# Kernel optimization log

Hardware: AMD Instinct MI355X
Metric: run time of the kernel (lower is better)

## Reference

```python
import jax, jax.numpy as jnp
import numpy as np

EMB = 64
NUM_LAYERS = 2


def _mlp_embed(x, shift, scale, w1, b1, w2, b2):
    # PreNormLayer: (x + shift) * scale, then Linear-ReLU-Linear-ReLU
    x = (x + shift) * scale
    x = jax.nn.relu(x @ w1 + b1)
    return jax.nn.relu(x @ w2 + b2)


def _sage_conv(x_src, x_dst, src_idx, dst_idx, ll_w, ll_b, lr_w):
    # PyG SAGEConv: mean-aggregate gathered source features at destinations,
    # out = lin_l(mean) + lin_r(x_dst); lin_l has bias, lin_r does not.
    n_dst = x_dst.shape[0]
    msgs = x_src[src_idx]                                   # [E, D] gather
    ssum = jax.ops.segment_sum(msgs, dst_idx, num_segments=n_dst)
    cnt = jax.ops.segment_sum(jnp.ones(src_idx.shape[0], x_src.dtype),
                              dst_idx, num_segments=n_dst)
    mean = ssum / jnp.maximum(cnt, 1.0)[:, None]            # [n_dst, D]
    return mean @ ll_w + ll_b + x_dst @ lr_w


def setup_inputs() -> dict:
    key = jax.random.key(0)
    ks = jax.random.split(key, 20)
    n_cons, n_var, n_edges = 100_000, 200_000, 2_000_000
    cons_nf, var_nf, edge_nf = 5, 19, 1

    def lin(k, fan_in, fan_out):
        return jax.random.normal(k, (fan_in, fan_out), jnp.float32) / np.sqrt(fan_in)

    inp = {
        'cons_x': jax.random.normal(ks[0], (n_cons, cons_nf), jnp.float32),
        'var_x': jax.random.normal(ks[1], (n_var, var_nf), jnp.float32),
        'edge_attr': jax.random.normal(ks[2], (n_edges, edge_nf), jnp.float32),
        'edge_index': jnp.stack([
            jax.random.randint(ks[3], (n_edges,), 0, n_cons),
            jax.random.randint(ks[4], (n_edges,), 0, n_var)]).astype(jnp.int64),
        # constraint embedding MLP
        'cons_shift': 0.1 * jax.random.normal(ks[5], (cons_nf,), jnp.float32),
        'cons_scale': 1.0 + 0.1 * jax.random.normal(ks[6], (cons_nf,), jnp.float32),
        'cons_w1': lin(ks[7], cons_nf, EMB),
        'cons_b1': jnp.zeros((EMB,), jnp.float32),
        'cons_w2': lin(ks[8], EMB, EMB),
        'cons_b2': jnp.zeros((EMB,), jnp.float32),
        # variable embedding MLP
        'var_shift': 0.1 * jax.random.normal(ks[9], (var_nf,), jnp.float32),
        'var_scale': 1.0 + 0.1 * jax.random.normal(ks[10], (var_nf,), jnp.float32),
        'var_w1': lin(ks[11], var_nf, EMB),
        'var_b1': jnp.zeros((EMB,), jnp.float32),
        'var_w2': lin(ks[12], EMB, EMB),
        'var_b2': jnp.zeros((EMB,), jnp.float32),
        # edge PreNorm (computed but unused for conv_type='sage', as in source)
        'edge_shift': 0.1 * jax.random.normal(ks[13], (edge_nf,), jnp.float32),
        'edge_scale': 1.0 + 0.1 * jax.random.normal(ks[14], (edge_nf,), jnp.float32),
        # SAGEConv weights: [layer, direction(0: cons->var, 1: var->cons), in, out]
        'conv_ll_w': jax.random.normal(ks[15], (NUM_LAYERS, 2, EMB, EMB), jnp.float32) / np.sqrt(EMB),
        'conv_ll_b': jnp.zeros((NUM_LAYERS, 2, EMB), jnp.float32),
        'conv_lr_w': jax.random.normal(ks[16], (NUM_LAYERS, 2, EMB, EMB), jnp.float32) / np.sqrt(EMB),
    }
    return inp


def reference(cons_x, var_x, edge_attr, edge_index,
              cons_shift, cons_scale, cons_w1, cons_b1, cons_w2, cons_b2,
              var_shift, var_scale, var_w1, var_b1, var_w2, var_b2,
              edge_shift, edge_scale, conv_ll_w, conv_ll_b, conv_lr_w):
    x_c = _mlp_embed(cons_x, cons_shift, cons_scale, cons_w1, cons_b1, cons_w2, cons_b2)
    x_v = _mlp_embed(var_x, var_shift, var_scale, var_w1, var_b1, var_w2, var_b2)
    edge_feat = (edge_attr + edge_shift) * edge_scale  # unused for SAGE (faithful to source)
    del edge_feat
    src, dst = edge_index[0], edge_index[1]  # constraint -> variable
    for l in range(NUM_LAYERS):
        new_v = _sage_conv(x_c, x_v, src, dst, conv_ll_w[l, 0], conv_ll_b[l, 0], conv_lr_w[l, 0])
        new_c = _sage_conv(x_v, x_c, dst, src, conv_ll_w[l, 1], conv_ll_b[l, 1], conv_lr_w[l, 1])
        x_c, x_v = jax.nn.relu(new_c), jax.nn.relu(new_v)
    return x_v
```

## Files before the change

kernel.cpp:

```cpp
#include <hip/hip_runtime.h>

#define EMB 64
#define CH 4096


static __device__ __forceinline__ unsigned short f2bf(float x) {
    union { float f; unsigned u; } v; v.f = x;
    unsigned r = v.u + 0x7fffu + ((v.u >> 16) & 1u);
    return (unsigned short)(r >> 16);
}
static __device__ __forceinline__ float bflo(unsigned w) {
    union { unsigned u; float f; } v; v.u = w << 16; return v.f;
}
static __device__ __forceinline__ float bfhi(unsigned w) {
    union { unsigned u; float f; } v; v.u = w & 0xffff0000u; return v.f;
}

__global__ __launch_bounds__(256) void zero_int_kernel(int* __restrict__ p, int n) {
    int i = blockIdx.x * 256 + threadIdx.x;
    if (i < n) p[i] = 0;
}

__global__ __launch_bounds__(256) void bucket_hist_kernel(
    const int* __restrict__ src, const int* __restrict__ dst, int E,
    int* __restrict__ bkt_cnt_c, int* __restrict__ bkt_cnt_v,
    int shc, int shv, int NBC, int NBV)
{
    __shared__ int hc[512], hv[512];
    int t = threadIdx.x;
    int base = blockIdx.x * CH;
    int n = min(CH, E - base);
    for (int i = t; i < NBC; i += 256) hc[i] = 0;
    for (int i = t; i < NBV; i += 256) hv[i] = 0;
    __syncthreads();
    for (int li = t; li < n; li += 256) {
        atomicAdd(&hc[src[base + li] >> shc], 1);
        atomicAdd(&hv[dst[base + li] >> shv], 1);
    }
    __syncthreads();
    for (int i = t; i < NBC; i += 256) { int c = hc[i]; if (c) atomicAdd(&bkt_cnt_c[i], c); }
    for (int i = t; i < NBV; i += 256) { int c = hv[i]; if (c) atomicAdd(&bkt_cnt_v[i], c); }
}

__global__ __launch_bounds__(256) void scan_buckets_kernel(
    int* __restrict__ bc, int nbc, int* __restrict__ bv, int nbv, int E)
{
    __shared__ int sc[256];
    int t = threadIdx.x;
    {
        int v0 = (2 * t < nbc) ? bc[2 * t] : 0;
        int v1 = (2 * t + 1 < nbc) ? bc[2 * t + 1] : 0;
        sc[t] = v0 + v1;
        __syncthreads();
        for (int off = 1; off < 256; off <<= 1) {
            int x = (t >= off) ? sc[t - off] : 0;
            __syncthreads();
            sc[t] += x;
            __syncthreads();
        }
        int ex = (t > 0) ? sc[t - 1] : 0;
        if (2 * t < nbc) bc[2 * t] = ex;
        if (2 * t + 1 < nbc) bc[2 * t + 1] = ex + v0;
        if (t == 0) bc[nbc] = E;
        __syncthreads();
    }
    {
        int v0 = (2 * t < nbv) ? bv[2 * t] : 0;
        int v1 = (2 * t + 1 < nbv) ? bv[2 * t + 1] : 0;
        sc[t] = v0 + v1;
        __syncthreads();
        for (int off = 1; off < 256; off <<= 1) {
            int x = (t >= off) ? sc[t - off] : 0;
            __syncthreads();
            sc[t] += x;
            __syncthreads();
        }
        int ex = (t > 0) ? sc[t - 1] : 0;
        if (2 * t < nbv) bv[2 * t] = ex;
        if (2 * t + 1 < nbv) bv[2 * t + 1] = ex + v0;
        if (t == 0) bv[nbv] = E;
    }
}

__global__ __launch_bounds__(256) void bin_edges_kernel(
    const int* __restrict__ src, const int* __restrict__ dst, int E,
    const int* __restrict__ bb_c, const int* __restrict__ bb_v,
    int* __restrict__ gcur_c, int* __restrict__ gcur_v,
    unsigned* __restrict__ tmp_c, unsigned* __restrict__ tmp_v,
    int shc, int shv, int NBC, int NBV)
{
    __shared__ int hc[512], hv[512];
    int t = threadIdx.x;
    int base = blockIdx.x * CH;
    int n = min(CH, E - base);
    unsigned mc = (1u << shc) - 1u, mv = (1u << shv) - 1u;

    for (int i = t; i < NBC; i += 256) hc[i] = 0;
    for (int i = t; i < NBV; i += 256) hv[i] = 0;
    __syncthreads();

    int ss[16], dd[16];
#pragma unroll
    for (int q = 0; q < 16; ++q) {
        int li = t + q * 256;
        bool ok = li < n;
        ss[q] = ok ? src[base + li] : -1;
        dd[q] = ok ? dst[base + li] : -1;
        if (ok) {
            atomicAdd(&hc[ss[q] >> shc], 1);
            atomicAdd(&hv[dd[q] >> shv], 1);
        }
    }
    __syncthreads();

    for (int i = t; i < NBC; i += 256) {
        int c = hc[i];
        hc[i] = c ? (bb_c[i] + atomicAdd(&gcur_c[i], c)) : 0;
    }
    for (int i = t; i < NBV; i += 256) {
        int c = hv[i];
        hv[i] = c ? (bb_v[i] + atomicAdd(&gcur_v[i], c)) : 0;
    }
    __syncthreads();

#pragma unroll
    for (int q = 0; q < 16; ++q) {
        int li = t + q * 256;
        if (li < n) {
            unsigned s = (unsigned)ss[q], d = (unsigned)dd[q];
            int pc = atomicAdd(&hc[s >> shc], 1);
            tmp_c[pc] = ((s & mc) << 23) | d;
            int pv = atomicAdd(&hv[d >> shv], 1);
            tmp_v[pv] = ((d & mv) << 23) | s;
        }
    }
}

__global__ __launch_bounds__(256) void regroup2_kernel(
    const unsigned* __restrict__ tmp, const int* __restrict__ bb,
    int* __restrict__ rp, int* __restrict__ adj, int n_nodes, int sh, int E, int nb)
{
    __shared__ int cnt[512];
    __shared__ int offs[512];
    __shared__ int sc[256];
    int t = threadIdx.x;
    int b = blockIdx.x;
    int node0 = b << sh;
    int node1 = min(node0 + (1 << sh), n_nodes);
    int nn = node1 - node0;
    for (int i = t; i < nn; i += 256) cnt[i] = 0;
    __syncthreads();
    int beg = bb[b], end = bb[b + 1];
    for (int e = beg + t; e < end; e += 256)
        atomicAdd(&cnt[tmp[e] >> 23], 1);
    __syncthreads();
    int v0 = (2 * t < nn) ? cnt[2 * t] : 0;
    int v1 = (2 * t + 1 < nn) ? cnt[2 * t + 1] : 0;
    sc[t] = v0 + v1;
    __syncthreads();
    for (int off = 1; off < 256; off <<= 1) {
        int x = (t >= off) ? sc[t - off] : 0;
        __syncthreads();
        sc[t] += x;
        __syncthreads();
    }
    int ex = (t > 0) ? sc[t - 1] : 0;
    if (2 * t < nn) offs[2 * t] = ex;
    if (2 * t + 1 < nn) offs[2 * t + 1] = ex + v0;
    __syncthreads();
    for (int i = t; i < nn; i += 256) {
        rp[node0 + i] = beg + offs[i];
        cnt[i] = 0;
    }
    if (b == nb - 1 && t == 0) rp[n_nodes] = E;
    __syncthreads();
    for (int e = beg + t; e < end; e += 256) {
        unsigned p = tmp[e];
        int d = (int)(p >> 23);
        int r = atomicAdd(&cnt[d], 1);
        adj[beg + offs[d] + r] = (int)(p & 0x7fffffu);
    }
}

template <int NF>
__global__ __launch_bounds__(256) void embed_fused_kernel(
    const float* __restrict__ x, const float* __restrict__ shift, const float* __restrict__ scale,
    const float* __restrict__ w1, const float* __restrict__ b1,
    const float* __restrict__ w2, const float* __restrict__ b2,
    const float* __restrict__ wll, const float* __restrict__ wlr,
    unsigned short* __restrict__ tb, float* __restrict__ u, int n)
{
    __shared__ float xs[NF * 68];
    __shared__ float w1s[NF * EMB];
    __shared__ float hs[EMB * 68];
    __shared__ float ws[EMB * EMB];
    __shared__ float b1s[EMB], b2s[EMB];

    int t = threadIdx.x;
    long row0 = (long)blockIdx.x * 64;
    int nrow = (int)((n - row0 < 64) ? (n - row0) : 64);

    for (int i = t; i < NF * EMB; i += 256) w1s[i] = w1[i];
    if (t < EMB) { b1s[t] = b1[t]; b2s[t] = b2[t]; }
    {
        const float4* wg = (const float4*)w2;
        float4* wl = (float4*)ws;
#pragma unroll
        for (int q = 0; q < 4; ++q) wl[t + q * 256] = wg[t + q * 256];
    }
    for (int i = t; i < 64 * NF; i += 256) {
        int r = i / NF, k = i - r * NF;
        float v = (r < nrow) ? x[row0 * NF + i] : 0.f;
        xs[k * 68 + r] = (v + shift[k]) * scale[k];
    }
    __syncthreads();

    int r0 = (t >> 4) * 4;
    int c0 = (t & 15) * 4;

    {
        float a1[4][4] = {{0.f}};
#pragma unroll
        for (int k = 0; k < NF; ++k) {
            float4 xv = *(const float4*)&xs[k * 68 + r0];
            float4 wv = *(const float4*)&w1s[k * EMB + c0];
            float xa[4] = {xv.x, xv.y, xv.z, xv.w};
            float wa[4] = {wv.x, wv.y, wv.z, wv.w};
#pragma unroll
            for (int i = 0; i < 4; ++i)
#pragma unroll
                for (int j = 0; j < 4; ++j)
                    a1[i][j] = fmaf(xa[i], wa[j], a1[i][j]);
        }
#pragma unroll
        for (int j = 0; j < 4; ++j) {
            float b = b1s[c0 + j];
            float4 o;
            o.x = fmaxf(a1[0][j] + b, 0.f);
            o.y = fmaxf(a1[1][j] + b, 0.f);
            o.z = fmaxf(a1[2][j] + b, 0.f);
            o.w = fmaxf(a1[3][j] + b, 0.f);
            *(float4*)&hs[(c0 + j) * 68 + r0] = o;
        }
    }
    __syncthreads();

    float a2[4][4] = {{0.f}};
#pragma unroll 8
    for (int k = 0; k < EMB; ++k) {
        float4 xv = *(const float4*)&hs[k * 68 + r0];
        float4 wv = *(const float4*)&ws[k * EMB + c0];
        float xa[4] = {xv.x, xv.y, xv.z, xv.w};
        float wa[4] = {wv.x, wv.y, wv.z, wv.w};
#pragma unroll
        for (int i = 0; i < 4; ++i)
#pragma unroll
            for (int j = 0; j < 4; ++j)
                a2[i][j] = fmaf(xa[i], wa[j], a2[i][j]);
    }
    __syncthreads();

#pragma unroll
    for (int j = 0; j < 4; ++j) {
        float b = b2s[c0 + j];
        float4 o;
        o.x = fmaxf(a2[0][j] + b, 0.f);
        o.y = fmaxf(a2[1][j] + b, 0.f);
        o.z = fmaxf(a2[2][j] + b, 0.f);
        o.w = fmaxf(a2[3][j] + b, 0.f);
        *(float4*)&hs[(c0 + j) * 68 + r0] = o;
    }
    {
        const float4* wg = (const float4*)wll;
        float4* wl = (float4*)ws;
#pragma unroll
        for (int q = 0; q < 4; ++q) wl[t + q * 256] = wg[t + q * 256];
    }
    __syncthreads();

    {
        float a3[4][4] = {{0.f}};
#pragma unroll 8
        for (int k = 0; k < EMB; ++k) {
            float4 xv = *(const float4*)&hs[k * 68 + r0];
            float4 wv = *(const float4*)&ws[k * EMB + c0];
            float xa[4] = {xv.x, xv.y, xv.z, xv.w};
            float wa[4] = {wv.x, wv.y, wv.z, wv.w};
#pragma unroll
            for (int i = 0; i < 4; ++i)
#pragma unroll
                for (int j = 0; j < 4; ++j)
                    a3[i][j] = fmaf(xa[i], wa[j], a3[i][j]);
        }
#pragma unroll
        for (int i = 0; i < 4; ++i) {
            long gr = row0 + r0 + i;
            if (gr < n) {
                ushort4 o;
                o.x = f2bf(a3[i][0]); o.y = f2bf(a3[i][1]);
                o.z = f2bf(a3[i][2]); o.w = f2bf(a3[i][3]);
                *(ushort4*)(tb + gr * EMB + c0) = o;
            }
        }
    }
    __syncthreads();

    {
        const float4* wg = (const float4*)wlr;
        float4* wl = (float4*)ws;
#pragma unroll
        for (int q = 0; q < 4; ++q) wl[t + q * 256] = wg[t + q * 256];
    }
    __syncthreads();

    {
        float a4[4][4] = {{0.f}};
#pragma unroll 8
        for (int k = 0; k < EMB; ++k) {
            float4 xv = *(const float4*)&hs[k * 68 + r0];
            float4 wv = *(const float4*)&ws[k * EMB + c0];
            float xa[4] = {xv.x, xv.y, xv.z, xv.w};
            float wa[4] = {wv.x, wv.y, wv.z, wv.w};
#pragma unroll
            for (int i = 0; i < 4; ++i)
#pragma unroll
                for (int j = 0; j < 4; ++j)
                    a4[i][j] = fmaf(xa[i], wa[j], a4[i][j]);
        }
#pragma unroll
        for (int i = 0; i < 4; ++i) {
            long gr = row0 + r0 + i;
            if (gr < n)
                *(float4*)&u[gr * EMB + c0] = make_float4(a4[i][0], a4[i][1], a4[i][2], a4[i][3]);
        }
    }
}

template <bool BF_OUT>
__global__ __launch_bounds__(512) void agg64_kernel(
    const unsigned short* __restrict__ tbl, const int* __restrict__ rowptr,
    const int* __restrict__ adj, const float* __restrict__ bias,
    const float* __restrict__ u, const float* __restrict__ W,
    void* __restrict__ outv, int n)
{
    __shared__ float xt[EMB * 68];
    __shared__ float ws[EMB * EMB];
    __shared__ float bs[EMB];

    int t = threadIdx.x;
    long node0 = (long)blockIdx.x * 64;
    int lane = t & 63;
    int wv = t >> 6;
    int p = lane & 15, g = lane >> 4;
    int f = 4 * p + g;

    {
        const float4* wg = (const float4*)W;
        float4* wl = (float4*)ws;
        wl[t] = wg[t];
        wl[t + 512] = wg[t + 512];
    }
    if (t < EMB) bs[t] = bias[t];
    __syncthreads();

    const uint2* tb = (const uint2*)tbl;
    for (int i = 0; i < 8; ++i) {
        int node = (int)node0 + wv * 8 + i;
        float val = 0.f;
        if (node < n) {
            int beg = rowptr[node];
            int end = rowptr[node + 1];
            float a0 = 0.f, a1 = 0.f, a2 = 0.f, a3 = 0.f;
            int e = beg + g;
            for (; e + 4 < end; e += 8) {
                int r0 = adj[e];
                int r1 = adj[e + 4];
                uint2 w0 = tb[(long)r0 * 16 + p];
                uint2 w1 = tb[(long)r1 * 16 + p];
                a0 += bflo(w0.x) + bflo(w1.x);
                a1 += bfhi(w0.x) + bfhi(w1.x);
                a2 += bflo(w0.y) + bflo(w1.y);
                a3 += bfhi(w0.y) + bfhi(w1.y);
            }
            if (e < end) {
                uint2 w0 = tb[(long)adj[e] * 16 + p];
                a0 += bflo(w0.x);
                a1 += bfhi(w0.x);
                a2 += bflo(w0.y);
                a3 += bfhi(w0.y);
            }
            a0 += __shfl_xor(a0, 16); a0 += __shfl_xor(a0, 32);
            a1 += __shfl_xor(a1, 16); a1 += __shfl_xor(a1, 32);
            a2 += __shfl_xor(a2, 16); a2 += __shfl_xor(a2, 32);
            a3 += __shfl_xor(a3, 16); a3 += __shfl_xor(a3, 32);
            int cnt = end - beg;
            float inv = 1.f / (float)(cnt > 0 ? cnt : 1);
            float av = (g == 0) ? a0 : ((g == 1) ? a1 : ((g == 2) ? a2 : a3));
            val = fmaxf(av * inv + bs[f] + u[(long)node * EMB + f], 0.f);
        }
        xt[f * 68 + (wv * 8 + i)] = val;
    }
    __syncthreads();

    int c0 = (t & 15) * 4;
    int r0 = (t >> 4) * 2;
    float acc[2][4] = {{0.f}};
#pragma unroll 8
    for (int k = 0; k < EMB; ++k) {
        float2 xv = *(const float2*)&xt[k * 68 + r0];
        float4 wv4 = *(const float4*)&ws[k * EMB + c0];
        float xa[2] = {xv.x, xv.y};
        float wa[4] = {wv4.x, wv4.y, wv4.z, wv4.w};
#pragma unroll
        for (int i = 0; i < 2; ++i)
#pragma unroll
            for (int j = 0; j < 4; ++j)
                acc[i][j] = fmaf(xa[i], wa[j], acc[i][j]);
    }
#pragma unroll
    for (int i = 0; i < 2; ++i) {
        long gr = node0 + r0 + i;
        if (gr < n) {
            if (BF_OUT) {
                ushort4 o;
                o.x = f2bf(acc[i][0]); o.y = f2bf(acc[i][1]);
                o.z = f2bf(acc[i][2]); o.w = f2bf(acc[i][3]);
                *(ushort4*)((unsigned short*)outv + gr * EMB + c0) = o;
            } else {
                *(float4*)((float*)outv + gr * EMB + c0) =
                    make_float4(acc[i][0], acc[i][1], acc[i][2], acc[i][3]);
            }
        }
    }
}

__global__ __launch_bounds__(256) void agg_bf16_kernel(
    const unsigned short* __restrict__ tbl, const int* __restrict__ rowptr,
    const int* __restrict__ adj, const float* __restrict__ bias,
    float* __restrict__ out, int n_dst)
{
    int lane = threadIdx.x & 63;
    int node = blockIdx.x * 4 + (threadIdx.x >> 6);
    if (node >= n_dst) return;
    int p = lane & 15;
    int g = lane >> 4;
    int beg = rowptr[node];
    int end = rowptr[node + 1];
    const uint2* tb = (const uint2*)tbl;
    float a0 = 0.f, a1 = 0.f, a2 = 0.f, a3 = 0.f;
    int e = beg + g;
    for (; e + 4 < end; e += 8) {
        int r0 = adj[e];
        int r1 = adj[e + 4];
        uint2 w0 = tb[(long)r0 * 16 + p];
        uint2 w1 = tb[(long)r1 * 16 + p];
        a0 += bflo(w0.x) + bflo(w1.x);
        a1 += bfhi(w0.x) + bfhi(w1.x);
        a2 += bflo(w0.y) + bflo(w1.y);
        a3 += bfhi(w0.y) + bfhi(w1.y);
    }
    if (e < end) {
        uint2 w0 = tb[(long)adj[e] * 16 + p];
        a0 += bflo(w0.x);
        a1 += bfhi(w0.x);
        a2 += bflo(w0.y);
        a3 += bfhi(w0.y);
    }
    a0 += __shfl_xor(a0, 16); a0 += __shfl_xor(a0, 32);
    a1 += __shfl_xor(a1, 16); a1 += __shfl_xor(a1, 32);
    a2 += __shfl_xor(a2, 16); a2 += __shfl_xor(a2, 32);
    a3 += __shfl_xor(a3, 16); a3 += __shfl_xor(a3, 32);
    if (g == 0) {
        int cnt = end - beg;
        float inv = 1.f / (float)(cnt > 0 ? cnt : 1);
        float4 bv = ((const float4*)bias)[p];
        float4* op = (float4*)(out + (long)node * EMB) + p;
        float4 ov = *op;
        float v0 = a0 * inv + bv.x + ov.x;
        float v1 = a1 * inv + bv.y + ov.y;
        float v2 = a2 * inv + bv.z + ov.z;
        float v3 = a3 * inv + bv.w + ov.w;
        *op = make_float4(fmaxf(v0, 0.f), fmaxf(v1, 0.f), fmaxf(v2, 0.f), fmaxf(v3, 0.f));
    }
}

extern "C" void kernel_launch(void* const* d_in, const int* in_sizes, int n_in,
                              void* d_out, int out_size, void* d_ws, size_t ws_size,
                              hipStream_t stream) {
    const float* cons_x     = (const float*)d_in[0];
    const float* var_x      = (const float*)d_in[1];
    const int*   eidx       = (const int*)d_in[3];
    const float* cons_shift = (const float*)d_in[4];
    const float* cons_scale = (const float*)d_in[5];
    const float* cons_w1    = (const float*)d_in[6];
    const float* cons_b1    = (const float*)d_in[7];
    const float* cons_w2    = (const float*)d_in[8];
    const float* cons_b2    = (const float*)d_in[9];
    const float* var_shift  = (const float*)d_in[10];
    const float* var_scale  = (const float*)d_in[11];
    const float* var_w1     = (const float*)d_in[12];
    const float* var_b1     = (const float*)d_in[13];
    const float* var_w2     = (const float*)d_in[14];
    const float* var_b2     = (const float*)d_in[15];
    const float* ll_w       = (const float*)d_in[18];
    const float* ll_b       = (const float*)d_in[19];
    const float* lr_w       = (const float*)d_in[20];

    const int nC = in_sizes[0] / 5;
    const int nV = in_sizes[1] / 19;
    const int E  = in_sizes[3] / 2;
    const int* src = eidx;
    const int* dst = eidx + E;

    int shc = 0; while ((nC >> shc) >= 512) ++shc;
    int shv = 0; while ((nV >> shv) >= 512) ++shv;
    const int NBC = (nC + (1 << shc) - 1) >> shc;
    const int NBV = (nV + (1 << shv) - 1) >> shv;

    char* w = (char*)d_ws;
    auto alloc = [&](size_t bytes) {
        char* p = w;
        w += (bytes + 255) & ~(size_t)255;
        return p;
    };
    float* x_c = (float*)alloc((size_t)nC * EMB * 4);
    float* x_v = (float*)alloc((size_t)nV * EMB * 4);
    float* t_c = (float*)alloc((size_t)nC * EMB * 4);
    float* t_v = (float*)alloc((size_t)nV * EMB * 4);
    unsigned* tmp_c = (unsigned*)t_c;
    unsigned* tmp_v = (unsigned*)t_v;
    unsigned short* tb_c = (unsigned short*)t_c;
    unsigned short* tb_v = (unsigned short*)t_v;
    int* rp_v  = (int*)alloc((size_t)(nV + 1) * 4);
    int* rp_c  = (int*)alloc((size_t)(nC + 1) * 4);
    int* adj_v = (int*)alloc((size_t)E * 4);
    int* adj_c = (int*)alloc((size_t)E * 4);
    int* bkt   = (int*)alloc(4096 * 4);
    int* bb_c   = bkt;
    int* bb_v   = bkt + 1024;
    int* gcur_c = bkt + 2048;
    int* gcur_v = bkt + 3072;

    auto llw = [&](int l, int d) { return ll_w + (size_t)(l * 2 + d) * EMB * EMB; };
    auto lrw = [&](int l, int d) { return lr_w + (size_t)(l * 2 + d) * EMB * EMB; };
    auto llb = [&](int l, int d) { return ll_b + (size_t)(l * 2 + d) * EMB; };

    zero_int_kernel<<<16, 256, 0, stream>>>(bkt, 4096);
    bucket_hist_kernel<<<(E + CH - 1) / CH, 256, 0, stream>>>(src, dst, E, bb_c, bb_v, shc, shv, NBC, NBV);
    scan_buckets_kernel<<<1, 256, 0, stream>>>(bb_c, NBC, bb_v, NBV, E);
    bin_edges_kernel<<<(E + CH - 1) / CH, 256, 0, stream>>>(src, dst, E, bb_c, bb_v, gcur_c, gcur_v,
                                                            tmp_c, tmp_v, shc, shv, NBC, NBV);
    regroup2_kernel<<<NBV, 256, 0, stream>>>(tmp_v, bb_v, rp_v, adj_v, nV, shv, E, NBV);
    regroup2_kernel<<<NBC, 256, 0, stream>>>(tmp_c, bb_c, rp_c, adj_c, nC, shc, E, NBC);

    embed_fused_kernel<5><<<(nC + 63) / 64, 256, 0, stream>>>(
        cons_x, cons_shift, cons_scale, cons_w1, cons_b1, cons_w2, cons_b2,
        llw(0, 0), lrw(0, 1), tb_c, x_c, nC);
    embed_fused_kernel<19><<<(nV + 63) / 64, 256, 0, stream>>>(
        var_x, var_shift, var_scale, var_w1, var_b1, var_w2, var_b2,
        llw(0, 1), lrw(0, 0), tb_v, x_v, nV);

    agg64_kernel<false><<<(nV + 63) / 64, 512, 0, stream>>>(
        tb_c, rp_v, adj_v, llb(0, 0), x_v, lrw(1, 0), d_out, nV);
    agg64_kernel<true><<<(nC + 63) / 64, 512, 0, stream>>>(
        tb_v, rp_c, adj_c, llb(0, 1), x_c, llw(1, 0), tb_c, nC);

    agg_bf16_kernel<<<(nV + 3) / 4, 256, 0, stream>>>(tb_c, rp_v, adj_v, llb(1, 0), (float*)d_out, nV);
}
```

Measured before the change: 480.3 us.

## Sort destination nodes by degree to balance aggregation work across waves

Adds a degree histogram and counting-sort pass that builds a per-side permutation of destination nodes grouped by in-degree. The aggregation kernels then process nodes in that order and scatter results to the original rows. The intent is to cut load imbalance inside blocks and waves. It also switches the shared-memory tile to a row-major layout with stride 65. The cost is extra preprocessing kernels and less locality in the u reads and output writes, which now follow the permutation.

```diff
diff --git a/kernel.cpp b/kernel.cpp
--- a/kernel.cpp
+++ b/kernel.cpp
@@ -2,6 +2,7 @@
 
 #define EMB 64
 #define CH 4096
+#define ST 65
 
 
 static __device__ __forceinline__ unsigned short f2bf(float x) {
@@ -182,6 +183,63 @@
     }
 }
 
+__global__ __launch_bounds__(256) void deg_hist_kernel(
+    const int* __restrict__ rp, int n, int* __restrict__ gbins)
+{
+    __shared__ int h[512];
+    int t = threadIdx.x;
+    for (int i = t; i < 512; i += 256) h[i] = 0;
+    __syncthreads();
+    int base = blockIdx.x * 2048;
+#pragma unroll
+    for (int q = 0; q < 8; ++q) {
+        int i = base + t + q * 256;
+        if (i < n) {
+            int deg = min(rp[i + 1] - rp[i], 511);
+            atomicAdd(&h[deg], 1);
+        }
+    }
+    __syncthreads();
+    for (int i = t; i < 512; i += 256) { int c = h[i]; if (c) atomicAdd(&gbins[i], c); }
+}
+
+__global__ __launch_bounds__(256) void deg_scatter_kernel(
+    const int* __restrict__ rp, int n, const int* __restrict__ bases,
+    int* __restrict__ cur, int* __restrict__ perm)
+{
+    __shared__ int h[512];
+    __shared__ int rb[512];
+    int t = threadIdx.x;
+    for (int i = t; i < 512; i += 256) h[i] = 0;
+    __syncthreads();
+    int base = blockIdx.x * 2048;
+    int dg[8];
+#pragma unroll
+    for (int q = 0; q < 8; ++q) {
+        int i = base + t + q * 256;
+        dg[q] = -1;
+        if (i < n) {
+            dg[q] = min(rp[i + 1] - rp[i], 511);
+            atomicAdd(&h[dg[q]], 1);
+        }
+    }
+    __syncthreads();
+    for (int i = t; i < 512; i += 256) {
+        int c = h[i];
+        rb[i] = c ? (bases[i] + atomicAdd(&cur[i], c)) : 0;
+        h[i] = 0;
+    }
+    __syncthreads();
+#pragma unroll
+    for (int q = 0; q < 8; ++q) {
+        int i = base + t + q * 256;
+        if (i < n) {
+            int r = atomicAdd(&h[dg[q]], 1);
+            perm[rb[dg[q]] + r] = i;
+        }
+    }
+}
+
 template <int NF>
 __global__ __launch_bounds__(256) void embed_fused_kernel(
     const float* __restrict__ x, const float* __restrict__ shift, const float* __restrict__ scale,
@@ -339,13 +397,14 @@
 template <bool BF_OUT>
 __global__ __launch_bounds__(512) void agg64_kernel(
     const unsigned short* __restrict__ tbl, const int* __restrict__ rowptr,
-    const int* __restrict__ adj, const float* __restrict__ bias,
-    const float* __restrict__ u, const float* __restrict__ W,
-    void* __restrict__ outv, int n)
-{
-    __shared__ float xt[EMB * 68];
+    const int* __restrict__ adj, const int* __restrict__ perm,
+    const float* __restrict__ bias, const float* __restrict__ u,
+    const float* __restrict__ W, void* __restrict__ outv, int n)
+{
+    __shared__ float xt[64 * ST];
     __shared__ float ws[EMB * EMB];
     __shared__ float bs[EMB];
+    __shared__ int nds[64];
 
     int t = threadIdx.x;
     long node0 = (long)blockIdx.x * 64;
@@ -361,13 +420,17 @@
         wl[t + 512] = wg[t + 512];
     }
     if (t < EMB) bs[t] = bias[t];
+    if (t < 64) nds[t] = (node0 + t < n) ? perm[node0 + t] : -1;
     __syncthreads();
 
     const uint2* tb = (const uint2*)tbl;
+    float bf = bs[f];
+#pragma unroll
     for (int i = 0; i < 8; ++i) {
-        int node = (int)node0 + wv * 8 + i;
+        int r = wv * 8 + i;
+        int node = nds[r];
         float val = 0.f;
-        if (node < n) {
+        if (node >= 0) {
             int beg = rowptr[node];
             int end = rowptr[node + 1];
             float a0 = 0.f, a1 = 0.f, a2 = 0.f, a3 = 0.f;
@@ -396,9 +459,9 @@
             int cnt = end - beg;
             float inv = 1.f / (float)(cnt > 0 ? cnt : 1);
             float av = (g == 0) ? a0 : ((g == 1) ? a1 : ((g == 2) ? a2 : a3));
-            val = fmaxf(av * inv + bs[f] + u[(long)node * EMB + f], 0.f);
-        }
-        xt[f * 68 + (wv * 8 + i)] = val;
+            val = fmaxf(av * inv + bf + u[(long)node * EMB + f], 0.f);
+        }
+        xt[r * ST + f] = val;
     }
     __syncthreads();
 
@@ -407,27 +470,29 @@
     float acc[2][4] = {{0.f}};
 #pragma unroll 8
     for (int k = 0; k < EMB; ++k) {
-        float2 xv = *(const float2*)&xt[k * 68 + r0];
+        float xa0 = xt[r0 * ST + k];
+        float xa1 = xt[(r0 + 1) * ST + k];
         float4 wv4 = *(const float4*)&ws[k * EMB + c0];
-        float xa[2] = {xv.x, xv.y};
-        float wa[4] = {wv4.x, wv4.y, wv4.z, wv4.w};
-#pragma unroll
-        for (int i = 0; i < 2; ++i)
-#pragma unroll
-            for (int j = 0; j < 4; ++j)
-                acc[i][j] = fmaf(xa[i], wa[j], acc[i][j]);
+        acc[0][0] = fmaf(xa0, wv4.x, acc[0][0]);
+        acc[0][1] = fmaf(xa0, wv4.y, acc[0][1]);
+        acc[0][2] = fmaf(xa0, wv4.z, acc[0][2]);
+        acc[0][3] = fmaf(xa0, wv4.w, acc[0][3]);
+        acc[1][0] = fmaf(xa1, wv4.x, acc[1][0]);
+        acc[1][1] = fmaf(xa1, wv4.y, acc[1][1]);
+        acc[1][2] = fmaf(xa1, wv4.z, acc[1][2]);
+        acc[1][3] = fmaf(xa1, wv4.w, acc[1][3]);
     }
 #pragma unroll
     for (int i = 0; i < 2; ++i) {
-        long gr = node0 + r0 + i;
-        if (gr < n) {
+        int node = nds[r0 + i];
+        if (node >= 0) {
             if (BF_OUT) {
                 ushort4 o;
                 o.x = f2bf(acc[i][0]); o.y = f2bf(acc[i][1]);
                 o.z = f2bf(acc[i][2]); o.w = f2bf(acc[i][3]);
-                *(ushort4*)((unsigned short*)outv + gr * EMB + c0) = o;
+                *(ushort4*)((unsigned short*)outv + (long)node * EMB + c0) = o;
             } else {
-                *(float4*)((float*)outv + gr * EMB + c0) =
+                *(float4*)((float*)outv + (long)node * EMB + c0) =
                     make_float4(acc[i][0], acc[i][1], acc[i][2], acc[i][3]);
             }
         }
@@ -436,12 +501,13 @@
 
 __global__ __launch_bounds__(256) void agg_bf16_kernel(
     const unsigned short* __restrict__ tbl, const int* __restrict__ rowptr,
-    const int* __restrict__ adj, const float* __restrict__ bias,
-    float* __restrict__ out, int n_dst)
+    const int* __restrict__ adj, const int* __restrict__ perm,
+    const float* __restrict__ bias, float* __restrict__ out, int n_dst)
 {
     int lane = threadIdx.x & 63;
-    int node = blockIdx.x * 4 + (threadIdx.x >> 6);
-    if (node >= n_dst) return;
+    int idx = blockIdx.x * 4 + (threadIdx.x >> 6);
+    if (idx >= n_dst) return;
+    int node = perm[idx];
     int p = lane & 15;
     int g = lane >> 4;
     int beg = rowptr[node];
@@ -535,17 +601,24 @@
     int* rp_c  = (int*)alloc((size_t)(nC + 1) * 4);
     int* adj_v = (int*)alloc((size_t)E * 4);
     int* adj_c = (int*)alloc((size_t)E * 4);
+    int* perm_v = (int*)alloc((size_t)nV * 4);
+    int* perm_c = (int*)alloc((size_t)nC * 4);
     int* bkt   = (int*)alloc(4096 * 4);
     int* bb_c   = bkt;
     int* bb_v   = bkt + 1024;
     int* gcur_c = bkt + 2048;
     int* gcur_v = bkt + 3072;
+    int* dsort  = (int*)alloc(4096 * 4);
+    int* bins_c = dsort;
+    int* bins_v = dsort + 1024;
+    int* dcur_c = dsort + 2048;
+    int* dcur_v = dsort + 3072;
 
     auto llw = [&](int l, int d) { return ll_w + (size_t)(l * 2 + d) * EMB * EMB; };
     auto lrw = [&](int l, int d) { return lr_w + (size_t)(l * 2 + d) * EMB * EMB; };
     auto llb = [&](int l, int d) { return ll_b + (size_t)(l * 2 + d) * EMB; };
 
-    zero_int_kernel<<<16, 256, 0, stream>>>(bkt, 4096);
+    zero_int_kernel<<<32, 256, 0, stream>>>(bkt, 8192);
     bucket_hist_kernel<<<(E + CH - 1) / CH, 256, 0, stream>>>(src, dst, E, bb_c, bb_v, shc, shv, NBC, NBV);
     scan_buckets_kernel<<<1, 256, 0, stream>>>(bb_c, NBC, bb_v, NBV, E);
     bin_edges_kernel<<<(E + CH - 1) / CH, 256, 0, stream>>>(src, dst, E, bb_c, bb_v, gcur_c, gcur_v,
@@ -553,6 +626,12 @@
     regroup2_kernel<<<NBV, 256, 0, stream>>>(tmp_v, bb_v, rp_v, adj_v, nV, shv, E, NBV);
     regroup2_kernel<<<NBC, 256, 0, stream>>>(tmp_c, bb_c, rp_c, adj_c, nC, shc, E, NBC);
 
+    deg_hist_kernel<<<(nV + 2047) / 2048, 256, 0, stream>>>(rp_v, nV, bins_v);
+    deg_hist_kernel<<<(nC + 2047) / 2048, 256, 0, stream>>>(rp_c, nC, bins_c);
+    scan_buckets_kernel<<<1, 256, 0, stream>>>(bins_c, 512, bins_v, 512, 0);
+    deg_scatter_kernel<<<(nV + 2047) / 2048, 256, 0, stream>>>(rp_v, nV, bins_v, dcur_v, perm_v);
+    deg_scatter_kernel<<<(nC + 2047) / 2048, 256, 0, stream>>>(rp_c, nC, bins_c, dcur_c, perm_c);
+
     embed_fused_kernel<5><<<(nC + 63) / 64, 256, 0, stream>>>(
         cons_x, cons_shift, cons_scale, cons_w1, cons_b1, cons_w2, cons_b2,
         llw(0, 0), lrw(0, 1), tb_c, x_c, nC);
@@ -561,9 +640,9 @@
         llw(0, 1), lrw(0, 0), tb_v, x_v, nV);
 
     agg64_kernel<false><<<(nV + 63) / 64, 512, 0, stream>>>(
-        tb_c, rp_v, adj_v, llb(0, 0), x_v, lrw(1, 0), d_out, nV);
+        tb_c, rp_v, adj_v, perm_v, llb(0, 0), x_v, lrw(1, 0), d_out, nV);
     agg64_kernel<true><<<(nC + 63) / 64, 512, 0, stream>>>(
-        tb_v, rp_c, adj_c, llb(0, 1), x_c, llw(1, 0), tb_c, nC);
-
-    agg_bf16_kernel<<<(nV + 3) / 4, 256, 0, stream>>>(tb_c, rp_v, adj_v, llb(1, 0), (float*)d_out, nV);
-}
+        tb_v, rp_c, adj_c, perm_c, llb(0, 1), x_c, llw(1, 0), tb_c, nC);
+
+    agg_bf16_kernel<<<(nV + 3) / 4, 256, 0, stream>>>(tb_c, rp_v, adj_v, perm_v, llb(1, 0), (float*)d_out, nV);
+}
```

New measurement: 515.3 us. 7.3% more time.

## Split fused aggregate+GEMM into separate aggregation and GEMM kernels

Applied to the files above, without the earlier changes.

Replaces the fused agg64 kernel, which gathered neighbours and then ran a 64x64 matmul in shared memory, with two separate passes. A per-node aggregation kernel now writes the relu'd layer-1 results in place, and a standalone 4x4-register-tiled GEMM kernel then produces the layer-2 projections. This aims to give the gather phase higher occupancy and a lighter per-node kernel. In exchange, the intermediate activations make an extra round trip through global memory and there are more kernel launches.

```diff
diff --git a/kernel.cpp b/kernel.cpp
--- a/kernel.cpp
+++ b/kernel.cpp
@@ -336,105 +336,77 @@
     }
 }
 
-template <bool BF_OUT>
-__global__ __launch_bounds__(512) void agg64_kernel(
-    const unsigned short* __restrict__ tbl, const int* __restrict__ rowptr,
-    const int* __restrict__ adj, const float* __restrict__ bias,
-    const float* __restrict__ u, const float* __restrict__ W,
-    void* __restrict__ outv, int n)
-{
-    __shared__ float xt[EMB * 68];
-    __shared__ float ws[EMB * EMB];
-    __shared__ float bs[EMB];
+template <bool BF1>
+__global__ __launch_bounds__(256) void gemm64_kernel(
+    const float* __restrict__ X, int n,
+    const float* __restrict__ W, void* __restrict__ Cv)
+{
+    __shared__ float xs[EMB * 68];
+    __shared__ float w1s[EMB * EMB];
 
     int t = threadIdx.x;
-    long node0 = (long)blockIdx.x * 64;
-    int lane = t & 63;
-    int wv = t >> 6;
-    int p = lane & 15, g = lane >> 4;
-    int f = 4 * p + g;
-
-    {
+    {
+        int r = t >> 2;
+        int cs = (t & 3) * 16;
+        long gr = (long)blockIdx.x * 64 + r;
+        float4 v[4];
+        if (gr < n) {
+            const float4* sp = (const float4*)(X + gr * EMB + cs);
+#pragma unroll
+            for (int q = 0; q < 4; ++q) v[q] = sp[q];
+        } else {
+            float4 z = make_float4(0.f, 0.f, 0.f, 0.f);
+#pragma unroll
+            for (int q = 0; q < 4; ++q) v[q] = z;
+        }
+#pragma unroll
+        for (int q = 0; q < 4; ++q) {
+            xs[(cs + q * 4 + 0) * 68 + r] = v[q].x;
+            xs[(cs + q * 4 + 1) * 68 + r] = v[q].y;
+            xs[(cs + q * 4 + 2) * 68 + r] = v[q].z;
+            xs[(cs + q * 4 + 3) * 68 + r] = v[q].w;
+        }
         const float4* wg = (const float4*)W;
-        float4* wl = (float4*)ws;
-        wl[t] = wg[t];
-        wl[t + 512] = wg[t + 512];
-    }
-    if (t < EMB) bs[t] = bias[t];
-    __syncthreads();
-
-    const uint2* tb = (const uint2*)tbl;
-    for (int i = 0; i < 8; ++i) {
-        int node = (int)node0 + wv * 8 + i;
-        float val = 0.f;
-        if (node < n) {
-            int beg = rowptr[node];
-            int end = rowptr[node + 1];
-            float a0 = 0.f, a1 = 0.f, a2 = 0.f, a3 = 0.f;
-            int e = beg + g;
-            for (; e + 4 < end; e += 8) {
-                int r0 = adj[e];
-                int r1 = adj[e + 4];
-                uint2 w0 = tb[(long)r0 * 16 + p];
-                uint2 w1 = tb[(long)r1 * 16 + p];
-                a0 += bflo(w0.x) + bflo(w1.x);
-                a1 += bfhi(w0.x) + bfhi(w1.x);
-                a2 += bflo(w0.y) + bflo(w1.y);
-                a3 += bfhi(w0.y) + bfhi(w1.y);
-            }
-            if (e < end) {
-                uint2 w0 = tb[(long)adj[e] * 16 + p];
-                a0 += bflo(w0.x);
-                a1 += bfhi(w0.x);
-                a2 += bflo(w0.y);
-                a3 += bfhi(w0.y);
-            }
-            a0 += __shfl_xor(a0, 16); a0 += __shfl_xor(a0, 32);
-            a1 += __shfl_xor(a1, 16); a1 += __shfl_xor(a1, 32);
-            a2 += __shfl_xor(a2, 16); a2 += __shfl_xor(a2, 32);
-            a3 += __shfl_xor(a3, 16); a3 += __shfl_xor(a3, 32);
-            int cnt = end - beg;
-            float inv = 1.f / (float)(cnt > 0 ? cnt : 1);
-            float av = (g == 0) ? a0 : ((g == 1) ? a1 : ((g == 2) ? a2 : a3));
-            val = fmaxf(av * inv + bs[f] + u[(long)node * EMB + f], 0.f);
-        }
-        xt[f * 68 + (wv * 8 + i)] = val;
-    }
-    __syncthreads();
-
+        float4* wl = (float4*)w1s;
+#pragma unroll
+        for (int q = 0; q < 4; ++q) wl[t + q * 256] = wg[t + q * 256];
+    }
+    __syncthreads();
+
+    int r0 = (t >> 4) * 4;
     int c0 = (t & 15) * 4;
-    int r0 = (t >> 4) * 2;
-    float acc[2][4] = {{0.f}};
+    float acc[4][4] = {{0.f}};
 #pragma unroll 8
     for (int k = 0; k < EMB; ++k) {
-        float2 xv = *(const float2*)&xt[k * 68 + r0];
-        float4 wv4 = *(const float4*)&ws[k * EMB + c0];
-        float xa[2] = {xv.x, xv.y};
-        float wa[4] = {wv4.x, wv4.y, wv4.z, wv4.w};
-#pragma unroll
-        for (int i = 0; i < 2; ++i)
+        float4 xv = *(const float4*)&xs[k * 68 + r0];
+        float4 wv = *(const float4*)&w1s[k * EMB + c0];
+        float xa[4] = {xv.x, xv.y, xv.z, xv.w};
+        float wa[4] = {wv.x, wv.y, wv.z, wv.w};
+#pragma unroll
+        for (int i = 0; i < 4; ++i)
 #pragma unroll
             for (int j = 0; j < 4; ++j)
                 acc[i][j] = fmaf(xa[i], wa[j], acc[i][j]);
     }
-#pragma unroll
-    for (int i = 0; i < 2; ++i) {
-        long gr = node0 + r0 + i;
+
+#pragma unroll
+    for (int i = 0; i < 4; ++i) {
+        long gr = (long)blockIdx.x * 64 + r0 + i;
         if (gr < n) {
-            if (BF_OUT) {
+            if (BF1) {
                 ushort4 o;
                 o.x = f2bf(acc[i][0]); o.y = f2bf(acc[i][1]);
                 o.z = f2bf(acc[i][2]); o.w = f2bf(acc[i][3]);
-                *(ushort4*)((unsigned short*)outv + gr * EMB + c0) = o;
+                *(ushort4*)((unsigned short*)Cv + gr * EMB + c0) = o;
             } else {
-                *(float4*)((float*)outv + gr * EMB + c0) =
+                *(float4*)((float*)Cv + gr * EMB + c0) =
                     make_float4(acc[i][0], acc[i][1], acc[i][2], acc[i][3]);
             }
         }
     }
 }
 
-__global__ __launch_bounds__(256) void agg_bf16_kernel(
+__global__ __launch_bounds__(256) void agg_rmw_kernel(
     const unsigned short* __restrict__ tbl, const int* __restrict__ rowptr,
     const int* __restrict__ adj, const float* __restrict__ bias,
     float* __restrict__ out, int n_dst)
@@ -560,10 +532,11 @@
         var_x, var_shift, var_scale, var_w1, var_b1, var_w2, var_b2,
         llw(0, 1), lrw(0, 0), tb_v, x_v, nV);
 
-    agg64_kernel<false><<<(nV + 63) / 64, 512, 0, stream>>>(
-        tb_c, rp_v, adj_v, llb(0, 0), x_v, lrw(1, 0), d_out, nV);
-    agg64_kernel<true><<<(nC + 63) / 64, 512, 0, stream>>>(
-        tb_v, rp_c, adj_c, llb(0, 1), x_c, llw(1, 0), tb_c, nC);
-
-    agg_bf16_kernel<<<(nV + 3) / 4, 256, 0, stream>>>(tb_c, rp_v, adj_v, llb(1, 0), (float*)d_out, nV);
-}
+    agg_rmw_kernel<<<(nV + 3) / 4, 256, 0, stream>>>(tb_c, rp_v, adj_v, llb(0, 0), x_v, nV);
+    agg_rmw_kernel<<<(nC + 3) / 4, 256, 0, stream>>>(tb_v, rp_c, adj_c, llb(0, 1), x_c, nC);
+
+    gemm64_kernel<true><<<(nC + 63) / 64, 256, 0, stream>>>(x_c, nC, llw(1, 0), tb_c);
+    gemm64_kernel<false><<<(nV + 63) / 64, 256, 0, stream>>>(x_v, nV, lrw(1, 0), d_out);
+
+    agg_rmw_kernel<<<(nV + 3) / 4, 256, 0, stream>>>(tb_c, rp_v, adj_v, llb(1, 0), (float*)d_out, nV);
+}
```

After: 488.8 us. Within noise of the previous version (+1.8%).
